# Performance work log

Hardware: AMD Instinct MI355X
Metric: run time of the kernel (lower is better)

The kernel has to match this reference:

```python
import jax, jax.numpy as jnp
import numpy as np

N, M, D = 131072, 2048, 2


def setup_inputs() -> dict:
    key = jax.random.key(0)
    k1, k2 = jax.random.split(key)
    sample = jax.random.normal(k1, (N, D), dtype=jnp.float32)
    mu = jax.random.uniform(k2, (M, D), dtype=jnp.float32)
    # A initialized as 15 * I per component, exactly as in the torch module
    A = (15.0 * jnp.broadcast_to(jnp.eye(D, dtype=jnp.float32), (M, D, D))).astype(jnp.float32)
    w = jnp.ones((M, 1), dtype=jnp.float32)
    return {"sample": sample, "mu": mu, "A": A, "w": w}


def reference(sample, mu, A, w):
    """GaussianMixture.log_likelihoods(sample): logsumexp_j( wlog_j - (x-mu_j)^T G_j (x-mu_j) )."""
    # update_covariances: G_m = A_m A_m^T / 2, shape (M, D, D)
    G = jnp.einsum('mij,mkj->mik', A, A) * 0.5
    g00, g01, g10, g11 = G[:, 0, 0], G[:, 0, 1], G[:, 1, 0], G[:, 1, 1]  # (M,)
    # covariances_determinants (2x2 case) + weights_log
    dets = g00 * g11 - g01 * g10                                          # (M,)
    wlog = jax.nn.log_softmax(w, axis=0)[:, 0] + 0.5 * jnp.log(dets)      # (M,)
    # Pairwise Mahalanobis quadratic form, D=2 expanded to avoid an (N,M,D) temp
    dx0 = sample[:, 0:1] - mu[None, :, 0]   # (N, M)
    dx1 = sample[:, 1:2] - mu[None, :, 1]   # (N, M)
    q = g00 * dx0 * dx0 + (g01 + g10) * dx0 * dx1 + g11 * dx1 * dx1       # (N, M)
    # mode='lse' reduction of kernel_product: log sum_j exp(wlog_j - q_ij)
    ll = jax.nn.logsumexp(wlog[None, :] - q, axis=1, keepdims=True)       # (N, 1)
    return ll
```

## Files before the change

kernel.cpp:

```cpp
#include <hip/hip_runtime.h>
#include <math.h>


#if __has_builtin(__builtin_amdgcn_exp2f)
#define EXP2(x) __builtin_amdgcn_exp2f(x)
#else
#define EXP2(x) exp2f(x)
#endif

typedef float v2f   __attribute__((ext_vector_type(2)));
typedef float f32x4 __attribute__((ext_vector_type(4)));
typedef short bf16x8 __attribute__((ext_vector_type(8)));
typedef float v4f __attribute__((ext_vector_type(4)));
typedef int   i4v __attribute__((ext_vector_type(4)));

#if __has_builtin(__builtin_elementwise_max)
#define VMAX(a, b) __builtin_elementwise_max(a, b)
#else
static __device__ inline v2f VMAX(v2f a, v2f b) {
  v2f r; r.x = fmaxf(a.x, b.x); r.y = fmaxf(a.y, b.y); return r;
}
static __device__ inline v4f VMAX(v4f a, v4f b) {
  v4f r; r.x = fmaxf(a.x, b.x); r.y = fmaxf(a.y, b.y);
  r.z = fmaxf(a.z, b.z); r.w = fmaxf(a.w, b.w); return r;
}
#endif

#define SCH_K1   8388608.0f
#define SCH_K2   1064986823.0f
#define SCH_TMIN 58353856.0f

#define SPLIT 8
#define CH  16
#define RMF 4
#define THR 40.0f
#define LOG2E 1.44269504088896340736f
#define LN2   0.69314718055994530942f

__device__ __forceinline__ unsigned short f2bf(float f) {
  unsigned u = __builtin_bit_cast(unsigned, f);
  unsigned r = u + 0x7FFFu + ((u >> 16) & 1u);
  return (unsigned short)(r >> 16);
}
__device__ __forceinline__ float bf2f(unsigned short h) {
  unsigned u = ((unsigned)h) << 16;
  return __builtin_bit_cast(float, u);
}

__device__ __forceinline__ float sch_e(float a, float knm) {
  const float u = fmaf(a, SCH_K1, knm);
  unsigned r;
  asm("v_cvt_u32_f32 %0, %1" : "=v"(r) : "v"(u));
  return __builtin_bit_cast(float, r);
}

__global__ __launch_bounds__(256) void prep_kernel(
    const float* __restrict__ mu,
    const float* __restrict__ A,
    const float* __restrict__ w,
    float* __restrict__ C,
    int M) {
  __shared__ float red[256];
  __shared__ int uni[256];
  const int t = threadIdx.x;

  float mx = -INFINITY;
  for (int m = t; m < M; m += 256) mx = fmaxf(mx, w[m]);
  red[t] = mx; __syncthreads();
  for (int s = 128; s > 0; s >>= 1) {
    if (t < s) red[t] = fmaxf(red[t], red[t + s]);
    __syncthreads();
  }
  const float wmax = red[0]; __syncthreads();

  float sum = 0.f;
  for (int m = t; m < M; m += 256) sum += expf(w[m] - wmax);
  red[t] = sum; __syncthreads();
  for (int s = 128; s > 0; s >>= 1) {
    if (t < s) red[t] += red[t + s];
    __syncthreads();
  }
  const float logZ = wmax + logf(red[0]);

  const float r00 = A[0], r01 = A[1], r10 = A[2], r11 = A[3];
  const float rg00 = 0.5f * (r00 * r00 + r01 * r01);
  const float rg01 = 0.5f * (r00 * r10 + r01 * r11);
  const float rg11 = 0.5f * (r10 * r10 + r11 * r11);

  unsigned short* Bp = (unsigned short*)(C + 6 * M + 16);

  int myuni = 1;
  for (int m = t; m < M; m += 256) {
    const float a00 = A[m * 4 + 0], a01 = A[m * 4 + 1];
    const float a10 = A[m * 4 + 2], a11 = A[m * 4 + 3];
    const float g00 = 0.5f * (a00 * a00 + a01 * a01);
    const float g01 = 0.5f * (a00 * a10 + a01 * a11);
    const float g11 = 0.5f * (a10 * a10 + a11 * a11);
    const float g01s = 2.0f * g01;
    const float det = g00 * g11 - g01 * g01;
    const float wlog = (w[m] - logZ) + 0.5f * logf(det);
    const float mu0 = mu[m * 2 + 0], mu1 = mu[m * 2 + 1];
    const float c0 = wlog - (g00 * mu0 * mu0 + g01s * mu0 * mu1 + g11 * mu1 * mu1);
    const float c2 = 2.0f * g00 * mu0 + g01s * mu1;
    const float c4 = 2.0f * g11 * mu1 + g01s * mu0;
    const float C0v = LOG2E * c0;
    const float C2v = LOG2E * c2;
    const float C4v = LOG2E * c4;
    C[0 * M + m] = C0v;
    C[1 * M + m] = LOG2E * -g00;
    C[2 * M + m] = C2v;
    C[3 * M + m] = LOG2E * -g11;
    C[4 * M + m] = C4v;
    C[5 * M + m] = LOG2E * -g01s;
    const unsigned short c2h = f2bf(C2v);
    const unsigned short c2l = f2bf(C2v - bf2f(c2h));
    const unsigned short c4h = f2bf(C4v);
    const unsigned short c4l = f2bf(C4v - bf2f(c4h));
    const unsigned short c0h = f2bf(C0v);
    const unsigned short c0l = f2bf(C0v - bf2f(c0h));
    Bp[m * 8 + 0] = c2h; Bp[m * 8 + 1] = c2h; Bp[m * 8 + 2] = c2l;
    Bp[m * 8 + 3] = c4h; Bp[m * 8 + 4] = c4h; Bp[m * 8 + 5] = c4l;
    Bp[m * 8 + 6] = c0h; Bp[m * 8 + 7] = c0l;
    myuni &= (g00 == rg00) & (g01 == rg01) & (g11 == rg11);
  }
  uni[t] = myuni; __syncthreads();
  for (int s = 128; s > 0; s >>= 1) {
    if (t < s) uni[t] &= uni[t + s];
    __syncthreads();
  }
  if (t == 0) {
    ((int*)C)[6 * M + 0] = uni[0];
    C[6 * M + 1] = LOG2E * -rg00;
    C[6 * M + 2] = LOG2E * -rg11;
    C[6 * M + 3] = LOG2E * -2.0f * rg01;
  }
}

#define MERGE(MXJ, SJ, OFF) do {                                             \
    const float om = __shfl_xor(MXJ, OFF, 64);                               \
    const float os = __shfl_xor(SJ, OFF, 64);                                \
    const float nm = fmaxf(MXJ, om);                                         \
    SJ = SJ * EXP2(MXJ - nm) + os * EXP2(om - nm);                           \
    MXJ = nm;                                                                \
  } while (0)

__global__ __launch_bounds__(512, 8) void gmix_mfma(
    const float2* __restrict__ xs,
    const float* __restrict__ C,
    float* __restrict__ out,
    int N, int M) {
  __shared__ float Lmx[SPLIT][2][64];
  __shared__ float Lsm[SPLIT][2][64];
  const int lane = threadIdx.x & 63;
  const int wave = __builtin_amdgcn_readfirstlane((int)(threadIdx.x >> 6));
  const int flag = ((const int*)C)[6 * M + 0];
  const float cb1 = C[6 * M + 1];
  const float cb3 = C[6 * M + 2];
  const float cb5 = C[6 * M + 3];

  if (flag) {
    const int sbase = blockIdx.x * 128 + wave * 16;
    const int col = lane & 15;
    const bf16x8* __restrict__ Bcol = (const bf16x8*)(C + 6 * M + 16) + col;

    const int sA = sbase + col;
    const float2 xa = (sA < N) ? xs[sA] : make_float2(0.f, 0.f);
    bf16x8 afrag = (bf16x8){0, 0, 0, 0, 0, 0, 0, 0};
    if (lane < 16) {
      const unsigned short x0h = f2bf(xa.x);
      const unsigned short x0l = f2bf(xa.x - bf2f(x0h));
      const unsigned short x1h = f2bf(xa.y);
      const unsigned short x1l = f2bf(xa.y - bf2f(x1h));
      afrag = (bf16x8){(short)x0h, (short)x0l, (short)x0h,
                       (short)x1h, (short)x1l, (short)x1h,
                       (short)0x3F80, (short)0x3F80};
    }

    float mx0 = -INFINITY, mx1 = -INFINITY, mx2 = -INFINITY, mx3 = -INFINITY;
    float s0 = 0.f, s1 = 0.f, s2 = 0.f, s3 = 0.f;
    float knm0 = 0.f, knm1 = 0.f, knm2 = 0.f, knm3 = 0.f;
    const f32x4 z4 = {0.f, 0.f, 0.f, 0.f};
    const int rounds = M / (RMF * 16);

    for (int t = 0; t < rounds; ++t) {
      f32x4 acc[RMF];
#pragma unroll
      for (int r = 0; r < RMF; ++r) {
        const bf16x8 bfrag = Bcol[t * (RMF * 16) + r * 16];
        acc[r] = __builtin_amdgcn_mfma_f32_16x16x32_bf16(afrag, bfrag, z4, 0, 0, 0);
      }
      const float cm0 = fmaxf(fmaxf(fmaxf(acc[0][0], acc[1][0]), acc[2][0]), acc[3][0]);
      const float cm1 = fmaxf(fmaxf(fmaxf(acc[0][1], acc[1][1]), acc[2][1]), acc[3][1]);
      const float cm2 = fmaxf(fmaxf(fmaxf(acc[0][2], acc[1][2]), acc[2][2]), acc[3][2]);
      const float cm3 = fmaxf(fmaxf(fmaxf(acc[0][3], acc[1][3]), acc[2][3]), acc[3][3]);
      const float d = fmaxf(fmaxf(cm0 - mx0, cm1 - mx1),
                            fmaxf(cm2 - mx2, cm3 - mx3));
      if (__any(d > THR)) {
#define RESC(J) do {                                                         \
          const float nm_ = fmaxf(mx##J, cm##J);                             \
          s##J *= EXP2(mx##J - nm_);                                         \
          mx##J = nm_;                                                       \
          knm##J = fmaf(nm_, -SCH_K1, SCH_K2);                               \
        } while (0)
        RESC(0); RESC(1); RESC(2); RESC(3);
#undef RESC
      }
#define EPIC(J) do {                                                         \
        const float e0 = sch_e(acc[0][J], knm##J);                           \
        const float e1 = sch_e(acc[1][J], knm##J);                           \
        const float e2 = sch_e(acc[2][J], knm##J);                           \
        const float e3 = sch_e(acc[3][J], knm##J);                           \
        s##J += (e0 + e1) + (e2 + e3);                                       \
      } while (0)
      EPIC(0); EPIC(1); EPIC(2); EPIC(3);
#undef EPIC
    }

#pragma unroll
    for (int off = 1; off < 16; off <<= 1) {
      MERGE(mx0, s0, off);
      MERGE(mx1, s1, off);
      MERGE(mx2, s2, off);
      MERGE(mx3, s3, off);
    }

    if (col == 0) {
      const int g = lane >> 4;
#define OUTJ(J, MXJ, SJ) do {                                                \
        const int sr = sbase + g * 4 + (J);                                  \
        if (sr < N) {                                                        \
          const float2 xo = xs[sr];                                          \
          const float base = cb1 * xo.x * xo.x + cb3 * xo.y * xo.y +         \
                             cb5 * xo.x * xo.y;                              \
          out[sr] = (MXJ + base + __log2f(SJ)) * LN2;                        \
        }                                                                    \
      } while (0)
      OUTJ(0, mx0, s0);
      OUTJ(1, mx1, s1);
      OUTJ(2, mx2, s2);
      OUTJ(3, mx3, s3);
#undef OUTJ
    }
  } else {
    const int nA = blockIdx.x * 128 + lane;
    const int nB = nA + 64;
    const float2 xA = (nA < N) ? xs[nA] : make_float2(0.f, 0.f);
    const float2 xB = (nB < N) ? xs[nB] : make_float2(0.f, 0.f);
    const v2f x0p = {xA.x, xB.x};
    const v2f x1p = {xA.y, xB.y};

    const int Mq = M / SPLIT;
    const int m0 = wave * Mq;
    const float* __restrict__ C0 = C + m0;
    const float* __restrict__ C1 = C + M + m0;
    const float* __restrict__ C2 = C + 2 * M + m0;
    const float* __restrict__ C3 = C + 3 * M + m0;
    const float* __restrict__ C4 = C + 4 * M + m0;
    const float* __restrict__ C5 = C + 5 * M + m0;

    v2f mx = {-INFINITY, -INFINITY};
    v2f sacc = {0.f, 0.f};
    for (int m = 0; m < Mq; m += CH) {
      v2f a[CH];
#pragma unroll
      for (int j = 0; j < CH; ++j) {
        const float c0 = C0[m + j], c1 = C1[m + j], c2 = C2[m + j];
        const float c3 = C3[m + j], c4 = C4[m + j], c5 = C5[m + j];
        v2f u = x0p * c1 + c2;
        u = x1p * c5 + u;
        v2f v = x1p * c3 + c4;
        v2f r = u * x0p + c0;
        a[j] = v * x1p + r;
      }
      v2f t0 = VMAX(a[0], a[1]);
      v2f t1 = VMAX(a[2], a[3]);
      v2f t2 = VMAX(a[4], a[5]);
      v2f t3 = VMAX(a[6], a[7]);
#pragma unroll
      for (int j = 8; j < CH; j += 4) {
        t0 = VMAX(t0, a[j]);     t1 = VMAX(t1, a[j + 1]);
        t2 = VMAX(t2, a[j + 2]); t3 = VMAX(t3, a[j + 3]);
      }
      const v2f cm = VMAX(VMAX(t0, t1), VMAX(t2, t3));
      const v2f nm = VMAX(mx, cm);
      v2f resc; resc.x = EXP2(mx.x - nm.x); resc.y = EXP2(mx.y - nm.y);
      v2f l0 = {0.f, 0.f}, l1 = {0.f, 0.f};
#pragma unroll
      for (int j = 0; j < CH; j += 2) {
        const v2f d0 = a[j] - nm, d1 = a[j + 1] - nm;
        v2f e0, e1;
        e0.x = EXP2(d0.x); e0.y = EXP2(d0.y);
        e1.x = EXP2(d1.x); e1.y = EXP2(d1.y);
        l0 += e0; l1 += e1;
      }
      sacc = sacc * resc + (l0 + l1);
      mx = nm;
    }
    const v2f base = cb1 * x0p * x0p + cb3 * x1p * x1p + cb5 * x0p * x1p;
#pragma unroll
    for (int k = 0; k < 2; ++k) {
      Lmx[wave][k][lane] = mx[k] + base[k];
      Lsm[wave][k][lane] = sacc[k];
    }
    __syncthreads();
    if (wave < 2) {
      const int n = blockIdx.x * 128 + wave * 64 + lane;
      if (n < N) {
        float gm = Lmx[0][wave][lane];
#pragma unroll
        for (int v = 1; v < SPLIT; ++v) gm = fmaxf(gm, Lmx[v][wave][lane]);
        float S = 0.f;
#pragma unroll
        for (int v = 0; v < SPLIT; ++v)
          S += Lsm[v][wave][lane] * EXP2(Lmx[v][wave][lane] - gm);
        out[n] = (gm + __log2f(S)) * LN2;
      }
    }
  }
}

__global__ __launch_bounds__(512, 4) void gmix_kernel(
    const float* __restrict__ sample,
    const float* __restrict__ C,
    float* __restrict__ out,
    int N, int M) {
  __shared__ float Lmx[SPLIT][4][64];
  __shared__ float Lsm[SPLIT][4][64];

  const int lane = threadIdx.x & 63;
  const int wave = __builtin_amdgcn_readfirstlane((int)(threadIdx.x >> 6));
  const int n0 = blockIdx.x * 256 + lane;

  float2 xs0 = (n0       < N) ? ((const float2*)sample)[n0      ] : make_float2(0.f, 0.f);
  float2 xs1 = (n0 + 64  < N) ? ((const float2*)sample)[n0 + 64 ] : make_float2(0.f, 0.f);
  float2 xs2 = (n0 + 128 < N) ? ((const float2*)sample)[n0 + 128] : make_float2(0.f, 0.f);
  float2 xs3 = (n0 + 192 < N) ? ((const float2*)sample)[n0 + 192] : make_float2(0.f, 0.f);
  const v4f x0q = {xs0.x, xs1.x, xs2.x, xs3.x};
  const v4f x1q = {xs0.y, xs1.y, xs2.y, xs3.y};

  const int flag = ((const int*)C)[6 * M + 0];
  const float cb1 = C[6 * M + 1];
  const float cb3 = C[6 * M + 2];
  const float cb5 = C[6 * M + 3];

  const int Mq = M / SPLIT;
  const int m0 = wave * Mq;
  const float* __restrict__ C0 = C + m0;
  const float* __restrict__ C1 = C + M + m0;
  const float* __restrict__ C2 = C + 2 * M + m0;
  const float* __restrict__ C3 = C + 3 * M + m0;
  const float* __restrict__ C4 = C + 4 * M + m0;
  const float* __restrict__ C5 = C + 5 * M + m0;

  v4f base4 = {0.f, 0.f, 0.f, 0.f};
  v4f mx = {-INFINITY, -INFINITY, -INFINITY, -INFINITY};
  v4f s  = {0.f, 0.f, 0.f, 0.f};
  const v4f tminv4 = {SCH_TMIN, SCH_TMIN, SCH_TMIN, SCH_TMIN};

  if (flag) {
    base4 = cb1 * x0q * x0q + cb3 * x1q * x1q + cb5 * x0q * x1q;
    for (int m = 0; m < Mq; m += CH) {
      v4f a[CH];
#pragma unroll
      for (int j = 0; j < CH; ++j) {
        const float c0 = C0[m + j], c2 = C2[m + j], c4 = C4[m + j];
        v4f t = x0q * c2 + c0;
        a[j] = x1q * c4 + t;
      }
      v4f t0 = VMAX(a[0], a[1]);
      v4f t1 = VMAX(a[2], a[3]);
      v4f t2 = VMAX(a[4], a[5]);
      v4f t3 = VMAX(a[6], a[7]);
#pragma unroll
      for (int j = 8; j < CH; j += 4) {
        t0 = VMAX(t0, a[j]);     t1 = VMAX(t1, a[j + 1]);
        t2 = VMAX(t2, a[j + 2]); t3 = VMAX(t3, a[j + 3]);
      }
      const v4f cm = VMAX(VMAX(t0, t1), VMAX(t2, t3));
      const v4f nm = VMAX(mx, cm);
      v4f resc;
      resc.x = EXP2(mx.x - nm.x); resc.y = EXP2(mx.y - nm.y);
      resc.z = EXP2(mx.z - nm.z); resc.w = EXP2(mx.w - nm.w);
      const v4f knm = SCH_K2 - nm * SCH_K1;
      v4f l0 = {0.f, 0.f, 0.f, 0.f}, l1 = {0.f, 0.f, 0.f, 0.f};
#pragma unroll
      for (int j = 0; j < CH; j += 2) {
        v4f u0 = a[j]     * SCH_K1 + knm;
        v4f u1 = a[j + 1] * SCH_K1 + knm;
        u0 = VMAX(u0, tminv4);
        u1 = VMAX(u1, tminv4);
        const i4v iv0 = __builtin_convertvector(u0, i4v);
        const i4v iv1 = __builtin_convertvector(u1, i4v);
        l0 += __builtin_bit_cast(v4f, iv0);
        l1 += __builtin_bit_cast(v4f, iv1);
      }
      s = s * resc + (l0 + l1);
      mx = nm;
    }
  } else {
    for (int m = 0; m < Mq; m += CH) {
      v4f a[CH];
#pragma unroll
      for (int j = 0; j < CH; ++j) {
        const float c0 = C0[m + j], c1 = C1[m + j], c2 = C2[m + j];
        const float c3 = C3[m + j], c4 = C4[m + j], c5 = C5[m + j];
        v4f u = x0q * c1 + c2;
        u = x1q * c5 + u;
        v4f v = x1q * c3 + c4;
        v4f r = u * x0q + c0;
        a[j] = v * x1q + r;
      }
      v4f t0 = VMAX(a[0], a[1]);
      v4f t1 = VMAX(a[2], a[3]);
      v4f t2 = VMAX(a[4], a[5]);
      v4f t3 = VMAX(a[6], a[7]);
#pragma unroll
      for (int j = 8; j < CH; j += 4) {
        t0 = VMAX(t0, a[j]);     t1 = VMAX(t1, a[j + 1]);
        t2 = VMAX(t2, a[j + 2]); t3 = VMAX(t3, a[j + 3]);
      }
      const v4f cm = VMAX(VMAX(t0, t1), VMAX(t2, t3));
      const v4f nm = VMAX(mx, cm);
      v4f resc;
      resc.x = EXP2(mx.x - nm.x); resc.y = EXP2(mx.y - nm.y);
      resc.z = EXP2(mx.z - nm.z); resc.w = EXP2(mx.w - nm.w);
      v4f l0 = {0.f, 0.f, 0.f, 0.f}, l1 = {0.f, 0.f, 0.f, 0.f};
#pragma unroll
      for (int j = 0; j < CH; j += 2) {
        v4f d0 = a[j] - nm, d1 = a[j + 1] - nm;
        v4f e0, e1;
        e0.x = EXP2(d0.x); e0.y = EXP2(d0.y); e0.z = EXP2(d0.z); e0.w = EXP2(d0.w);
        e1.x = EXP2(d1.x); e1.y = EXP2(d1.y); e1.z = EXP2(d1.z); e1.w = EXP2(d1.w);
        l0 += e0; l1 += e1;
      }
      s = s * resc + (l0 + l1);
      mx = nm;
    }
  }

#pragma unroll
  for (int k = 0; k < 4; ++k) {
    Lmx[wave][k][lane] = mx[k] + base4[k];
    Lsm[wave][k][lane] = s[k];
  }
  __syncthreads();

  if (wave < 4) {
    const int set = wave;
    const int n = blockIdx.x * 256 + set * 64 + lane;
    if (n < N) {
      float gm = Lmx[0][set][lane];
#pragma unroll
      for (int v = 1; v < SPLIT; ++v) gm = fmaxf(gm, Lmx[v][set][lane]);
      float S = 0.f;
#pragma unroll
      for (int v = 0; v < SPLIT; ++v)
        S += Lsm[v][set][lane] * EXP2(Lmx[v][set][lane] - gm);
      out[n] = (gm + __log2f(S)) * LN2;
    }
  }
}

extern "C" void kernel_launch(void* const* d_in, const int* in_sizes, int n_in,
                              void* d_out, int out_size, void* d_ws, size_t ws_size,
                              hipStream_t stream) {
  const float* sample = (const float*)d_in[0];
  const float* mu     = (const float*)d_in[1];
  const float* A      = (const float*)d_in[2];
  const float* w      = (const float*)d_in[3];
  float* out = (float*)d_out;

  const int N = in_sizes[0] / 2;
  const int M = in_sizes[3];

  float* C = (float*)d_ws;
  const size_t need = ((size_t)6 * M + 16) * 4 + (size_t)M * 16;

  prep_kernel<<<1, 256, 0, stream>>>(mu, A, w, C, M);

  if (ws_size >= need && M % (RMF * 16) == 0 && M % (SPLIT * CH) == 0) {
    gmix_mfma<<<(N + 127) / 128, 512, 0, stream>>>(
        (const float2*)sample, C, out, N, M);
  } else {
    gmix_kernel<<<(N + 255) / 256, 512, 0, stream>>>(sample, C, out, N, M);
  }
}
```

Baseline: 111.8 us.

## Parallelize prep kernel across blocks and vectorize MFMA epilogue with packed v2f ops

The single-block prep kernel is split so block 0 computes the weight log-normalizer and uniformity flag while the other blocks build the per-component coefficient tables in parallel. The log-normalizer is no longer folded into each component's constant and is instead subtracted once per sample in the final output. The MFMA path's max and exp-accumulate epilogue is rewritten with two-wide float vectors so the compiler can emit packed FP32 instructions. This shortens the serial prep stage at the cost of an extra workspace read and a slightly different floating-point rounding order.

```diff
diff --git a/kernel.cpp b/kernel.cpp
--- a/kernel.cpp
+++ b/kernel.cpp
@@ -25,6 +25,9 @@
   r.z = fmaxf(a.z, b.z); r.w = fmaxf(a.w, b.w); return r;
 }
 #endif
+
+#define LO2(v) __builtin_shufflevector((v), (v), 0, 1)
+#define HI2(v) __builtin_shufflevector((v), (v), 2, 3)
 
 #define SCH_K1   8388608.0f
 #define SCH_K2   1064986823.0f
@@ -47,8 +50,7 @@
   return __builtin_bit_cast(float, u);
 }
 
-__device__ __forceinline__ float sch_e(float a, float knm) {
-  const float u = fmaf(a, SCH_K1, knm);
+__device__ __forceinline__ float sch_cvt(float u) {
   unsigned r;
   asm("v_cvt_u32_f32 %0, %1" : "=v"(r) : "v"(u));
   return __builtin_bit_cast(float, r);
@@ -60,37 +62,62 @@
     const float* __restrict__ w,
     float* __restrict__ C,
     int M) {
-  __shared__ float red[256];
-  __shared__ int uni[256];
   const int t = threadIdx.x;
 
-  float mx = -INFINITY;
-  for (int m = t; m < M; m += 256) mx = fmaxf(mx, w[m]);
-  red[t] = mx; __syncthreads();
-  for (int s = 128; s > 0; s >>= 1) {
-    if (t < s) red[t] = fmaxf(red[t], red[t + s]);
-    __syncthreads();
-  }
-  const float wmax = red[0]; __syncthreads();
-
-  float sum = 0.f;
-  for (int m = t; m < M; m += 256) sum += expf(w[m] - wmax);
-  red[t] = sum; __syncthreads();
-  for (int s = 128; s > 0; s >>= 1) {
-    if (t < s) red[t] += red[t + s];
-    __syncthreads();
-  }
-  const float logZ = wmax + logf(red[0]);
-
-  const float r00 = A[0], r01 = A[1], r10 = A[2], r11 = A[3];
-  const float rg00 = 0.5f * (r00 * r00 + r01 * r01);
-  const float rg01 = 0.5f * (r00 * r10 + r01 * r11);
-  const float rg11 = 0.5f * (r10 * r10 + r11 * r11);
+  if (blockIdx.x == 0) {
+    __shared__ float red[256];
+    __shared__ int uni[256];
+
+    float mx = -INFINITY;
+    for (int m = t; m < M; m += 256) mx = fmaxf(mx, w[m]);
+    red[t] = mx; __syncthreads();
+    for (int s = 128; s > 0; s >>= 1) {
+      if (t < s) red[t] = fmaxf(red[t], red[t + s]);
+      __syncthreads();
+    }
+    const float wmax = red[0]; __syncthreads();
+
+    float sum = 0.f;
+    for (int m = t; m < M; m += 256) sum += expf(w[m] - wmax);
+    red[t] = sum; __syncthreads();
+    for (int s = 128; s > 0; s >>= 1) {
+      if (t < s) red[t] += red[t + s];
+      __syncthreads();
+    }
+    const float logZ = wmax + logf(red[0]);
+
+    const float r00 = A[0], r01 = A[1], r10 = A[2], r11 = A[3];
+    const float rg00 = 0.5f * (r00 * r00 + r01 * r01);
+    const float rg01 = 0.5f * (r00 * r10 + r01 * r11);
+    const float rg11 = 0.5f * (r10 * r10 + r11 * r11);
+
+    int myuni = 1;
+    for (int m = t; m < M; m += 256) {
+      const float a00 = A[m * 4 + 0], a01 = A[m * 4 + 1];
+      const float a10 = A[m * 4 + 2], a11 = A[m * 4 + 3];
+      const float g00 = 0.5f * (a00 * a00 + a01 * a01);
+      const float g01 = 0.5f * (a00 * a10 + a01 * a11);
+      const float g11 = 0.5f * (a10 * a10 + a11 * a11);
+      myuni &= (g00 == rg00) & (g01 == rg01) & (g11 == rg11);
+    }
+    uni[t] = myuni; __syncthreads();
+    for (int s = 128; s > 0; s >>= 1) {
+      if (t < s) uni[t] &= uni[t + s];
+      __syncthreads();
+    }
+    if (t == 0) {
+      ((int*)C)[6 * M + 0] = uni[0];
+      C[6 * M + 1] = LOG2E * -rg00;
+      C[6 * M + 2] = LOG2E * -rg11;
+      C[6 * M + 3] = LOG2E * -2.0f * rg01;
+      C[6 * M + 4] = LOG2E * logZ;
+    }
+    return;
+  }
 
   unsigned short* Bp = (unsigned short*)(C + 6 * M + 16);
-
-  int myuni = 1;
-  for (int m = t; m < M; m += 256) {
+  const int nwb = (int)gridDim.x - 1;
+  for (int m = ((int)blockIdx.x - 1) * 256 + t; m < M; m += nwb * 256) {
     const float a00 = A[m * 4 + 0], a01 = A[m * 4 + 1];
     const float a10 = A[m * 4 + 2], a11 = A[m * 4 + 3];
     const float g00 = 0.5f * (a00 * a00 + a01 * a01);
@@ -98,7 +125,7 @@
     const float g11 = 0.5f * (a10 * a10 + a11 * a11);
     const float g01s = 2.0f * g01;
     const float det = g00 * g11 - g01 * g01;
-    const float wlog = (w[m] - logZ) + 0.5f * logf(det);
+    const float wlog = w[m] + 0.5f * logf(det);
     const float mu0 = mu[m * 2 + 0], mu1 = mu[m * 2 + 1];
     const float c0 = wlog - (g00 * mu0 * mu0 + g01s * mu0 * mu1 + g11 * mu1 * mu1);
     const float c2 = 2.0f * g00 * mu0 + g01s * mu1;
@@ -121,18 +148,6 @@
     Bp[m * 8 + 0] = c2h; Bp[m * 8 + 1] = c2h; Bp[m * 8 + 2] = c2l;
     Bp[m * 8 + 3] = c4h; Bp[m * 8 + 4] = c4h; Bp[m * 8 + 5] = c4l;
     Bp[m * 8 + 6] = c0h; Bp[m * 8 + 7] = c0l;
-    myuni &= (g00 == rg00) & (g01 == rg01) & (g11 == rg11);
-  }
-  uni[t] = myuni; __syncthreads();
-  for (int s = 128; s > 0; s >>= 1) {
-    if (t < s) uni[t] &= uni[t + s];
-    __syncthreads();
-  }
-  if (t == 0) {
-    ((int*)C)[6 * M + 0] = uni[0];
-    C[6 * M + 1] = LOG2E * -rg00;
-    C[6 * M + 2] = LOG2E * -rg11;
-    C[6 * M + 3] = LOG2E * -2.0f * rg01;
   }
 }
 
@@ -157,6 +172,7 @@
   const float cb1 = C[6 * M + 1];
   const float cb3 = C[6 * M + 2];
   const float cb5 = C[6 * M + 3];
+  const float logZh = C[6 * M + 4];
 
   if (flag) {
     const int sbase = blockIdx.x * 128 + wave * 16;
@@ -176,9 +192,9 @@
                        (short)0x3F80, (short)0x3F80};
     }
 
-    float mx0 = -INFINITY, mx1 = -INFINITY, mx2 = -INFINITY, mx3 = -INFINITY;
-    float s0 = 0.f, s1 = 0.f, s2 = 0.f, s3 = 0.f;
-    float knm0 = 0.f, knm1 = 0.f, knm2 = 0.f, knm3 = 0.f;
+    v2f mx01 = {-INFINITY, -INFINITY}, mx23 = {-INFINITY, -INFINITY};
+    v2f s01 = {0.f, 0.f}, s23 = {0.f, 0.f};
+    v2f knm01 = {0.f, 0.f}, knm23 = {0.f, 0.f};
     const f32x4 z4 = {0.f, 0.f, 0.f, 0.f};
     const int rounds = M / (RMF * 16);
 
@@ -189,32 +205,37 @@
         const bf16x8 bfrag = Bcol[t * (RMF * 16) + r * 16];
         acc[r] = __builtin_amdgcn_mfma_f32_16x16x32_bf16(afrag, bfrag, z4, 0, 0, 0);
       }
-      const float cm0 = fmaxf(fmaxf(fmaxf(acc[0][0], acc[1][0]), acc[2][0]), acc[3][0]);
-      const float cm1 = fmaxf(fmaxf(fmaxf(acc[0][1], acc[1][1]), acc[2][1]), acc[3][1]);
-      const float cm2 = fmaxf(fmaxf(fmaxf(acc[0][2], acc[1][2]), acc[2][2]), acc[3][2]);
-      const float cm3 = fmaxf(fmaxf(fmaxf(acc[0][3], acc[1][3]), acc[2][3]), acc[3][3]);
-      const float d = fmaxf(fmaxf(cm0 - mx0, cm1 - mx1),
-                            fmaxf(cm2 - mx2, cm3 - mx3));
-      if (__any(d > THR)) {
-#define RESC(J) do {                                                         \
-          const float nm_ = fmaxf(mx##J, cm##J);                             \
-          s##J *= EXP2(mx##J - nm_);                                         \
-          mx##J = nm_;                                                       \
-          knm##J = fmaf(nm_, -SCH_K1, SCH_K2);                               \
-        } while (0)
-        RESC(0); RESC(1); RESC(2); RESC(3);
-#undef RESC
-      }
-#define EPIC(J) do {                                                         \
-        const float e0 = sch_e(acc[0][J], knm##J);                           \
-        const float e1 = sch_e(acc[1][J], knm##J);                           \
-        const float e2 = sch_e(acc[2][J], knm##J);                           \
-        const float e3 = sch_e(acc[3][J], knm##J);                           \
-        s##J += (e0 + e1) + (e2 + e3);                                       \
-      } while (0)
-      EPIC(0); EPIC(1); EPIC(2); EPIC(3);
-#undef EPIC
-    }
+      const v2f cm01 = VMAX(VMAX(LO2(acc[0]), LO2(acc[1])),
+                            VMAX(LO2(acc[2]), LO2(acc[3])));
+      const v2f cm23 = VMAX(VMAX(HI2(acc[0]), HI2(acc[1])),
+                            VMAX(HI2(acc[2]), HI2(acc[3])));
+      const v2f dp = VMAX(cm01 - mx01, cm23 - mx23);
+      const float dmax = fmaxf(dp.x, dp.y);
+      if (__any(dmax > THR)) {
+        const v2f nm01 = VMAX(mx01, cm01);
+        const v2f nm23 = VMAX(mx23, cm23);
+        v2f r01, r23;
+        r01.x = EXP2(mx01.x - nm01.x); r01.y = EXP2(mx01.y - nm01.y);
+        r23.x = EXP2(mx23.x - nm23.x); r23.y = EXP2(mx23.y - nm23.y);
+        s01 *= r01; s23 *= r23;
+        mx01 = nm01; mx23 = nm23;
+        knm01 = SCH_K2 - nm01 * SCH_K1;
+        knm23 = SCH_K2 - nm23 * SCH_K1;
+      }
+#pragma unroll
+      for (int r = 0; r < RMF; ++r) {
+        const v2f u01 = LO2(acc[r]) * SCH_K1 + knm01;
+        const v2f u23 = HI2(acc[r]) * SCH_K1 + knm23;
+        v2f e01, e23;
+        e01.x = sch_cvt(u01.x); e01.y = sch_cvt(u01.y);
+        e23.x = sch_cvt(u23.x); e23.y = sch_cvt(u23.y);
+        s01 += e01;
+        s23 += e23;
+      }
+    }
+
+    float mx0 = mx01.x, mx1 = mx01.y, mx2 = mx23.x, mx3 = mx23.y;
+    float s0 = s01.x, s1 = s01.y, s2 = s23.x, s3 = s23.y;
 
 #pragma unroll
     for (int off = 1; off < 16; off <<= 1) {
@@ -231,7 +252,7 @@
         if (sr < N) {                                                        \
           const float2 xo = xs[sr];                                          \
           const float base = cb1 * xo.x * xo.x + cb3 * xo.y * xo.y +         \
-                             cb5 * xo.x * xo.y;                              \
+                             cb5 * xo.x * xo.y - logZh;                      \
           out[sr] = (MXJ + base + __log2f(SJ)) * LN2;                        \
         }                                                                    \
       } while (0)
@@ -296,7 +317,8 @@
       sacc = sacc * resc + (l0 + l1);
       mx = nm;
     }
-    const v2f base = cb1 * x0p * x0p + cb3 * x1p * x1p + cb5 * x0p * x1p;
+    const v2f base = cb1 * x0p * x0p + cb3 * x1p * x1p + cb5 * x0p * x1p
+                     - (v2f){logZh, logZh};
 #pragma unroll
     for (int k = 0; k < 2; ++k) {
       Lmx[wave][k][lane] = mx[k] + base[k];
@@ -342,6 +364,7 @@
   const float cb1 = C[6 * M + 1];
   const float cb3 = C[6 * M + 2];
   const float cb5 = C[6 * M + 3];
+  const float logZh = C[6 * M + 4];
 
   const int Mq = M / SPLIT;
   const int m0 = wave * Mq;
@@ -356,9 +379,10 @@
   v4f mx = {-INFINITY, -INFINITY, -INFINITY, -INFINITY};
   v4f s  = {0.f, 0.f, 0.f, 0.f};
   const v4f tminv4 = {SCH_TMIN, SCH_TMIN, SCH_TMIN, SCH_TMIN};
+  const v4f logZ4 = {logZh, logZh, logZh, logZh};
 
   if (flag) {
-    base4 = cb1 * x0q * x0q + cb3 * x1q * x1q + cb5 * x0q * x1q;
+    base4 = cb1 * x0q * x0q + cb3 * x1q * x1q + cb5 * x0q * x1q - logZ4;
     for (int m = 0; m < Mq; m += CH) {
       v4f a[CH];
 #pragma unroll
@@ -398,6 +422,7 @@
       mx = nm;
     }
   } else {
+    base4 = cb1 * x0q * x0q + cb3 * x1q * x1q + cb5 * x0q * x1q - logZ4;
     for (int m = 0; m < Mq; m += CH) {
       v4f a[CH];
 #pragma unroll
@@ -476,7 +501,8 @@
   float* C = (float*)d_ws;
   const size_t need = ((size_t)6 * M + 16) * 4 + (size_t)M * 16;
 
-  prep_kernel<<<1, 256, 0, stream>>>(mu, A, w, C, M);
+  const int prepBlocks = 1 + (M + 255) / 256;
+  prep_kernel<<<prepBlocks, 256, 0, stream>>>(mu, A, w, C, M);
 
   if (ws_size >= need && M % (RMF * 16) == 0 && M % (SPLIT * CH) == 0) {
     gmix_mfma<<<(N + 127) / 128, 512, 0, stream>>>(
```

New measurement: 111.7 us. About the same (-0.0%).
